# Kernel optimization log

Measured on AMD Instinct MI355X. Metric: run time of the kernel, lower is better.

## Reference

```python
import jax, jax.numpy as jnp
import numpy as np

HIDDEN = 64
EF_DIM = 3
RBOUND = 10.0
GROUP = 5
NEXP_MEAN = 0.05   # fixed normalization constants of the 'nexpnorm' RBF
NEXP_STD = 0.15
COORDS_WEIGHT = 1.0
N_NODES = 100000
N_GRAPHS = N_NODES // GROUP


def act(x):
    return jax.nn.relu(x)


def rbf(dist, num_rbf):
    # ExpNormal smearing with cosine cutoff (non-trainable), then fixed normalization.
    # dist: (..., 1) -> (..., num_rbf)
    alpha = 5.0 / RBOUND
    start = float(np.exp(-RBOUND))
    means = jnp.linspace(start, 1.0, num_rbf).astype(dist.dtype)
    beta = (2.0 / num_rbf * (1.0 - start)) ** -2
    cutoff = 0.5 * (jnp.cos(dist * jnp.pi / RBOUND) + 1.0) * (dist <= RBOUND)
    r = cutoff * jnp.exp(-beta * (jnp.exp(-alpha * dist) - means) ** 2)
    return (r - NEXP_MEAN) / NEXP_STD


def safe_pdist(a, b):
    # pairwise L2 norm (B,G,1,3)-(B,1,G,3) -> (B,G,G,1); grad-safe at zero
    d = a[:, :, None, :] - b[:, None, :, :]
    sq = jnp.sum(d * d, axis=-1, keepdims=True)
    return jnp.sqrt(jnp.where(sq == 0.0, 1.0, sq)) * (sq > 0.0)


def mlp2(x, w1, b1, w2, b2):
    return act(act(x @ w1 + b1) @ w2 + b2)


def mixed_wl(row, col, coord, vel, ic_wef, ic_pat, br_w1, br_b1, br_w2, br_b2, out_w, out_b):
    B = coord.shape[0] // GROUP
    c = coord.reshape(B, GROUP, 3)
    v = vel.reshape(B, GROUP, 3)
    mcd = safe_pdist(c, v)  # mixed coord-vel distances
    ef = jnp.concatenate([
        rbf(safe_pdist(c, c), EF_DIM),
        rbf(safe_pdist(v, v), EF_DIM),
        rbf(mcd, EF_DIM),
        rbf(jnp.swapaxes(mcd, 1, 2), EF_DIM),
    ], axis=-1)  # (B, 5, 5, 4*EF_DIM)
    # TwoFDisInit: linear embed * pattern embedding (diag tuples get pattern id 2, off-diag 1)
    idx = jnp.arange(GROUP)
    pattern = jnp.ones((GROUP, GROUP), dtype=jnp.int32).at[idx, idx].set(2)
    kemb = (ef @ ic_wef) * ic_pat[pattern]  # (B, 5, 5, H)
    # TwoFDisLayer (color_steps = 1): three branch MLPs, matrix-multiply mixing, residual add
    sm = mlp2(kemb, br_w1[0], br_b1[0], br_w2[0], br_b2[0])
    k0 = mlp2(kemb, br_w1[1], br_b1[1], br_w2[1], br_b2[1])
    k1 = mlp2(kemb, br_w1[2], br_b1[2], br_w2[2], br_b2[2])
    mult = jnp.einsum('bijd,bjkd->bikd', k0, k1)
    kemb = kemb + act((sm * mult) @ out_w + out_b)
    # gather per-edge tuple embedding
    return kemb[row // GROUP, row % GROUP, col % GROUP]  # (E, H)


def setup_inputs():
    key = jax.random.key(0)
    ks = jax.random.split(key, 20)
    N, H = N_NODES, HIDDEN
    # fully-connected (no self loops) edges inside each 5-node graph
    pairs = np.array([(i, j) for i in range(GROUP) for j in range(GROUP) if i != j])
    off = np.arange(N_GRAPHS) * GROUP
    row = (off[:, None] + pairs[None, :, 0]).reshape(-1)
    col = (off[:, None] + pairs[None, :, 1]).reshape(-1)
    edge_index = jnp.asarray(np.stack([row, col]), dtype=jnp.int32)
    g = lambda k, shp, s=0.05: jax.random.normal(k, shp, dtype=jnp.float32) * s
    return {
        'h': g(ks[0], (N, H), 0.5),
        'coord': g(ks[1], (N, 3), 1.0),
        'vel': g(ks[2], (N, 3), 1.0),
        'edge_index': edge_index,
        'e_w1': g(ks[3], (2 * H + 1 + H, H)), 'e_b1': jnp.zeros((H,), jnp.float32),
        'e_w2': g(ks[4], (H, H)), 'e_b2': jnp.zeros((H,), jnp.float32),
        'n_w1': g(ks[5], (2 * H, H)), 'n_b1': jnp.zeros((H,), jnp.float32),
        'n_w2': g(ks[6], (H, H)), 'n_b2': jnp.zeros((H,), jnp.float32),
        'c_w1': g(ks[7], (H, H)), 'c_b1': jnp.zeros((H,), jnp.float32),
        'c_w2': g(ks[8], (H, 1), 0.001),  # xavier gain=0.001, bias-free
        'v_w1': g(ks[9], (H, H)), 'v_b1': jnp.zeros((H,), jnp.float32),
        'v_w2': g(ks[10], (H, 1)), 'v_b2': jnp.zeros((1,), jnp.float32),
        'ic_wef': g(ks[11], (4 * EF_DIM, H), 0.1),
        'ic_pat': g(ks[12], (3, H), 0.1),
        'br_w1': g(ks[13], (3, H, H)), 'br_b1': jnp.zeros((3, H), jnp.float32),
        'br_w2': g(ks[14], (3, H, H)), 'br_b2': jnp.zeros((3, H), jnp.float32),
        'out_w': g(ks[15], (H, H)), 'out_b': jnp.zeros((H,), jnp.float32),
    }


def reference(h, coord, vel, edge_index, e_w1, e_b1, e_w2, e_b2, n_w1, n_b1, n_w2, n_b2,
              c_w1, c_b1, c_w2, v_w1, v_b1, v_w2, v_b2, ic_wef, ic_pat,
              br_w1, br_b1, br_w2, br_b2, out_w, out_b):
    row, col = edge_index[0], edge_index[1]
    N = h.shape[0]
    # coord2radial (norm_diff=False)
    coord_diff = coord[row] - coord[col]                      # (E, 3)
    radial = jnp.sum(coord_diff * coord_diff, axis=1, keepdims=True)  # (E, 1)
    # mixed 2-WL tuple embedding per edge
    kemb = mixed_wl(row, col, coord, vel, ic_wef, ic_pat, br_w1, br_b1, br_w2, br_b2, out_w, out_b)
    # edge model (attention=False)
    edge_feat = mlp2(jnp.concatenate([h[row], h[col], radial, kemb], axis=1),
                     e_w1, e_b1, e_w2, e_b2)                  # (E, H)
    # coord model: per-edge scalar (num_vectors_in=out=1), clamp, segment mean
    cmat = act(edge_feat @ c_w1 + c_b1) @ c_w2                # (E, 1)
    trans = jnp.clip(coord_diff * cmat, -100.0, 100.0)        # (E, 3)
    cnt = jax.ops.segment_sum(jnp.ones((row.shape[0],), trans.dtype), row, num_segments=N)
    agg = jax.ops.segment_sum(trans, row, num_segments=N) / jnp.maximum(cnt, 1.0)[:, None]
    # velocity update: coord += coord_mlp_vel(h) * vel
    vmat = act(h @ v_w1 + v_b1) @ v_w2 + v_b2                 # (N, 1)
    coord_out = (coord + agg * COORDS_WEIGHT + vel * vmat)[:, :, None]  # (N, 3, 1)
    # node model (recurrent=True)
    nagg = jax.ops.segment_sum(edge_feat, row, num_segments=N)
    h_out = h + (act(jnp.concatenate([h, nagg], axis=1) @ n_w1 + n_b1) @ n_w2 + n_b2)
    return h_out, coord_out
```

## Files before the change

### kernel.cpp

```cpp
#include <hip/hip_runtime.h>
#include <math.h>

#define HD 64
#define WPB 2

typedef unsigned short u16;
typedef unsigned int u32;
typedef __attribute__((ext_vector_type(8))) short short8;
typedef __attribute__((ext_vector_type(4))) float f32x4;

__device__ __forceinline__ u16 f2bf(float f) {
  u32 r;
  asm("v_cvt_pk_bf16_f32 %0, %1, %2" : "=v"(r) : "v"(f), "v"(f));
  return (u16)r;
}
__device__ __forceinline__ u32 pk2(float lo, float hi) {
  u32 r;
  asm("v_cvt_pk_bf16_f32 %0, %1, %2" : "=v"(r) : "v"(lo), "v"(hi));
  return r;
}
__device__ __forceinline__ float bf2f(u16 x) {
  return __uint_as_float(((u32)x) << 16);
}
__device__ __forceinline__ int uswz(int row, int col) {
  return (row << 6) | (col ^ (((row >> 2) & 3) << 4));
}
__device__ __forceinline__ float rlane(float v, int l) {
  return __uint_as_float(__builtin_amdgcn_readlane(__float_as_uint(v), l));
}
__device__ __forceinline__ void fence() {
  asm volatile("s_waitcnt lgkmcnt(0)" ::: "memory");
}

template <int MT, int RMAX>
__device__ __forceinline__ void loadA(const u16* A_, int t, short8* a0, short8* a1) {
  const int q8 = (t >> 4) << 3;
#pragma unroll
  for (int mt = 0; mt < MT; ++mt) {
    int row = mt * 16 + (t & 15);
    row = row > RMAX ? RMAX : row;
    const int idx = uswz(row, q8);
    a0[mt] = *reinterpret_cast<const short8*>(A_ + idx);
    a1[mt] = *reinterpret_cast<const short8*>(A_ + (idx ^ 32));
  }
}

template <int MTT>
__device__ __forceinline__ void mmh(const short8* a0, const short8* a1,
                                    const u16* __restrict__ WT, f32x4 (*acc)[2],
                                    int t, int nh) {
  const int c15 = t & 15;
  const int q8 = (t >> 4) << 3;
  short8 b[2][2];
#pragma unroll
  for (int n2 = 0; n2 < 2; ++n2) {
    const int nt = nh * 2 + n2;
#pragma unroll
    for (int s = 0; s < 2; ++s)
      b[n2][s] = *reinterpret_cast<const short8*>(WT + (nt * 16 + c15) * 64 + s * 32 + q8);
  }
#pragma unroll
  for (int mt = 0; mt < MTT; ++mt) {
#pragma unroll
    for (int n2 = 0; n2 < 2; ++n2)
      acc[mt][n2] = __builtin_amdgcn_mfma_f32_16x16x32_bf16(a0[mt], b[n2][0], acc[mt][n2], 0, 0, 0);
#pragma unroll
    for (int n2 = 0; n2 < 2; ++n2)
      acc[mt][n2] = __builtin_amdgcn_mfma_f32_16x16x32_bf16(a1[mt], b[n2][1], acc[mt][n2], 0, 0, 0);
  }
}

template <int MT, int RMAX, int EPI>
__device__ __forceinline__ void run_phase2(const u16* AA, const u16* AB,
                                           u16* DA, u16* DB,
                                           const u16* MA, const u16* MB,
                                           const u16* __restrict__ WT,
                                           const float* __restrict__ bias,
                                           int t, int rowoff = 0) {
  const int c15 = t & 15, q = t >> 4;
  constexpr int rowlim = (MT == 2) ? 25 : 5;
  short8 a0[2 * MT], a1[2 * MT];
  loadA<MT, RMAX>(AA, t, a0, a1);
  loadA<MT, RMAX>(AB, t, a0 + MT, a1 + MT);
#pragma unroll
  for (int nh = 0; nh < 2; ++nh) {
    f32x4 acc[2 * MT][2];
#pragma unroll
    for (int n2 = 0; n2 < 2; ++n2) {
      const int col = (nh * 2 + n2) * 16 + c15;
      const float bb = bias ? bias[col] : 0.0f;
#pragma unroll
      for (int mt = 0; mt < 2 * MT; ++mt) acc[mt][n2] = (f32x4){bb, bb, bb, bb};
    }
    mmh<2 * MT>(a0, a1, WT, acc, t, nh);
#pragma unroll
    for (int n2 = 0; n2 < 2; ++n2) {
      const int col = (nh * 2 + n2) * 16 + c15;
#pragma unroll
      for (int mt = 0; mt < 2 * MT; ++mt) {
        u16* D_ = (mt < MT) ? DA : DB;
        const u16* M_ = (mt < MT) ? MA : MB;
        const int r0 = (mt % MT) * 16 + q * 4;
        const int bix = uswz(r0 + rowoff, col);
#pragma unroll
        for (int i = 0; i < 4; ++i) {
          if (r0 + i < rowlim) {
            const int ix = bix + i * 64;
            float v = acc[mt][n2][i];
            if (EPI >= 2) v = fmaxf(v, 0.0f);
            if (EPI == 3) v *= bf2f(M_[ix]);
            if (EPI == 4) v += bf2f(D_[ix]);
            D_[ix] = f2bf(v);
          }
        }
      }
    }
  }
}

__global__ __launch_bounds__(256) void prepack(
    const float* __restrict__ br_w1, const float* __restrict__ br_w2,
    const float* __restrict__ out_w, const float* __restrict__ e_w1,
    const float* __restrict__ e_w2, const float* __restrict__ c_w1,
    const float* __restrict__ v_w1, const float* __restrict__ n_w1,
    const float* __restrict__ n_w2, const float* __restrict__ ic_wef,
    u16* __restrict__ W) {
  const int m = blockIdx.x;
  if (m == 16) {
    for (int e = threadIdx.x; e < 2048; e += blockDim.x) {
      const int n = e >> 5, k = e & 31;
      W[16 * 4096 + e] = (k < 12) ? f2bf(ic_wef[k * 64 + n]) : (u16)0;
    }
    return;
  }
  const float* src;
  switch (m) {
    case 0: src = br_w1; break;
    case 1: src = br_w1 + 4096; break;
    case 2: src = br_w1 + 8192; break;
    case 3: src = br_w2; break;
    case 4: src = br_w2 + 4096; break;
    case 5: src = br_w2 + 8192; break;
    case 6: src = out_w; break;
    case 7: src = e_w1; break;
    case 8: src = e_w1 + 64 * 64; break;
    case 9: src = e_w1 + 129 * 64; break;
    case 10: src = e_w2; break;
    case 11: src = c_w1; break;
    case 12: src = v_w1; break;
    case 13: src = n_w1; break;
    case 14: src = n_w1 + 64 * 64; break;
    default: src = n_w2; break;
  }
  u16* dst = W + m * 4096;
  for (int e = threadIdx.x; e < 4096; e += blockDim.x) {
    const int n = e >> 6, k = e & 63;
    dst[e] = f2bf(src[k * 64 + n]);
  }
}

__global__ __launch_bounds__(64 * WPB, 2) void egcl_mfma(
    const float* __restrict__ gh, const float* __restrict__ gcoord,
    const float* __restrict__ gvel, const u16* __restrict__ Wg,
    const float* __restrict__ e_w1, const float* __restrict__ e_b1,
    const float* __restrict__ e_b2,
    const float* __restrict__ n_b1, const float* __restrict__ n_b2,
    const float* __restrict__ c_b1, const float* __restrict__ c_w2,
    const float* __restrict__ v_b1, const float* __restrict__ v_w2,
    const float* __restrict__ v_b2,
    const float* __restrict__ ic_pat,
    const float* __restrict__ br_b1, const float* __restrict__ br_b2,
    const float* __restrict__ out_b,
    float* __restrict__ hout, float* __restrict__ cout, int B) {
  __shared__ __align__(16) u16 arena[WPB][9600];

  const int t = threadIdx.x & 63;
  const int wv = threadIdx.x >> 6;
  const int gA = (blockIdx.x * WPB + wv) * 2;
  if (gA >= B) return;
  int gB = gA + 1;
  if (gB >= B) gB = gA;

  u16* AR = arena[wv];
  u16* KA = AR;           u16* KB = AR + 1600;
  u16* TA = AR + 3200;    u16* TB = AR + 4800;
  u16* UA = AR + 6400;    u16* UB = AR + 8000;
  u16* EFa = TA;
  u16* EFb = TB;
  const int c15 = t & 15, q = t >> 4, q8 = q << 3;
#define WT(m) (Wg + (m) * 4096)

  short8 hA0, hA1;
  {
    int nd = c15 & 7;
    nd = nd > 4 ? 4 : nd;
    const int gg = (c15 & 8) ? gB : gA;
    const float* hp = gh + (size_t)(gg * 5 + nd) * HD + q8;
    const float4 f0 = *reinterpret_cast<const float4*>(hp);
    const float4 f1 = *reinterpret_cast<const float4*>(hp + 4);
    const float4 f2 = *reinterpret_cast<const float4*>(hp + 32);
    const float4 f3 = *reinterpret_cast<const float4*>(hp + 36);
    union { u32 w[4]; short8 s; } u0, u1;
    u0.w[0] = pk2(f0.x, f0.y); u0.w[1] = pk2(f0.z, f0.w);
    u0.w[2] = pk2(f1.x, f1.y); u0.w[3] = pk2(f1.z, f1.w);
    u1.w[0] = pk2(f2.x, f2.y); u1.w[1] = pk2(f2.z, f2.w);
    u1.w[2] = pk2(f3.x, f3.y); u1.w[3] = pk2(f3.z, f3.w);
    hA0 = u0.s;
    hA1 = u1.s;
  }

  float scvreg = 0.0f;
  if (t < 15) scvreg = gcoord[gA * 15 + t];
  else if (t >= 16 && t < 31) scvreg = gvel[gA * 15 + (t - 16)];
  else if (t >= 32 && t < 47) scvreg = gcoord[gB * 15 + (t - 32)];
  else if (t >= 48 && t < 63) scvreg = gvel[gB * 15 + (t - 48)];

#pragma unroll
  for (int z = 0; z < 8; ++z) {
    const int e = t + z * 64;
    if (e < 500) {
      const int gsel = e >= 250;
      const int ee = e - gsel * 250;
      const int row = ee / 10, cc = 12 + (ee % 10) * 2;
      *reinterpret_cast<u32*>((gsel ? EFb : EFa) + row * 32 + cc) = 0u;
    }
  }

  float sqcc = 0.0f;
  {
    const int lb = (t >= 32) ? 32 : 0;
    const int tt = t - lb;
    if (tt < 25) {
      u16* EF = lb ? EFb : EFa;
      const int ti = tt / 5, tj = tt % 5;
      const float cix = __shfl(scvreg, lb + ti * 3 + 0, 64), ciy = __shfl(scvreg, lb + ti * 3 + 1, 64), ciz = __shfl(scvreg, lb + ti * 3 + 2, 64);
      const float cjx = __shfl(scvreg, lb + tj * 3 + 0, 64), cjy = __shfl(scvreg, lb + tj * 3 + 1, 64), cjz = __shfl(scvreg, lb + tj * 3 + 2, 64);
      const float vix = __shfl(scvreg, lb + 16 + ti * 3 + 0, 64), viy = __shfl(scvreg, lb + 16 + ti * 3 + 1, 64), viz = __shfl(scvreg, lb + 16 + ti * 3 + 2, 64);
      const float vjx = __shfl(scvreg, lb + 16 + tj * 3 + 0, 64), vjy = __shfl(scvreg, lb + 16 + tj * 3 + 1, 64), vjz = __shfl(scvreg, lb + 16 + tj * 3 + 2, 64);
      {
        const float dx = cix - cjx, dy = ciy - cjy, dz = ciz - cjz;
        sqcc = dx * dx + dy * dy + dz * dz;
      }
      auto sd = [](float sq) { return (sq > 0.0f) ? sqrtf(sq) : 0.0f; };
      float sq2;
      const float dcc = sd(sqcc);
      {
        const float dx = vix - vjx, dy = viy - vjy, dz = viz - vjz;
        sq2 = dx * dx + dy * dy + dz * dz;
      }
      const float dvv = sd(sq2);
      {
        const float dx = cix - vjx, dy = ciy - vjy, dz = ciz - vjz;
        sq2 = dx * dx + dy * dy + dz * dz;
      }
      const float dcv = sd(sq2);
      {
        const float dx = cjx - vix, dy = cjy - viy, dz = cjz - viz;
        sq2 = dx * dx + dy * dy + dz * dz;
      }
      const float dvc = sd(sq2);
      auto rbf3 = [&](float d, int base) {
        const float cut = (d <= 10.0f) ? (0.5f * (cosf(d * 0.31415926535897931f) + 1.0f)) : 0.0f;
        const float e = expf(-0.5f * d);
        const float u0 = e - 4.5399929762484854e-05f;
        const float u1 = e - 0.50002270f;
        const float u2 = e - 1.0f;
        const float BETA = 2.2502043f;
        EF[tt * 32 + base + 0] = f2bf((cut * expf(-BETA * u0 * u0) - 0.05f) * (1.0f / 0.15f));
        EF[tt * 32 + base + 1] = f2bf((cut * expf(-BETA * u1 * u1) - 0.05f) * (1.0f / 0.15f));
        EF[tt * 32 + base + 2] = f2bf((cut * expf(-BETA * u2 * u2) - 0.05f) * (1.0f / 0.15f));
      };
      rbf3(dcc, 0);
      rbf3(dvv, 3);
      rbf3(dcv, 6);
      rbf3(dvc, 9);
    }
  }
  fence();

  {
    short8 aE[4];
#pragma unroll
    for (int gsel = 0; gsel < 2; ++gsel) {
      const u16* EF = gsel ? EFb : EFa;
#pragma unroll
      for (int mt = 0; mt < 2; ++mt) {
        int row = mt * 16 + c15;
        row = row > 24 ? 24 : row;
        aE[gsel * 2 + mt] = *reinterpret_cast<const short8*>(EF + row * 32 + q8);
      }
    }
    const u16* WTp = Wg + 16 * 4096;
#pragma unroll
    for (int nh = 0; nh < 2; ++nh) {
      f32x4 acc[4][2];
#pragma unroll
      for (int mt = 0; mt < 4; ++mt)
#pragma unroll
        for (int n2 = 0; n2 < 2; ++n2) acc[mt][n2] = (f32x4){0.f, 0.f, 0.f, 0.f};
      short8 b[2];
#pragma unroll
      for (int n2 = 0; n2 < 2; ++n2)
        b[n2] = *reinterpret_cast<const short8*>(WTp + ((nh * 2 + n2) * 16 + c15) * 32 + q8);
#pragma unroll
      for (int mt = 0; mt < 4; ++mt)
#pragma unroll
        for (int n2 = 0; n2 < 2; ++n2)
          acc[mt][n2] = __builtin_amdgcn_mfma_f32_16x16x32_bf16(aE[mt], b[n2], acc[mt][n2], 0, 0, 0);
#pragma unroll
      for (int n2 = 0; n2 < 2; ++n2) {
        const int col = (nh * 2 + n2) * 16 + c15;
        const float p1 = ic_pat[64 + col], p2 = ic_pat[128 + col];
#pragma unroll
        for (int mt = 0; mt < 4; ++mt) {
          u16* K_ = (mt < 2) ? KA : KB;
          const int r0 = (mt & 1) * 16 + q * 4;
          const int bix = uswz(r0, col);
#pragma unroll
          for (int i = 0; i < 4; ++i) {
            const int row = r0 + i;
            if (row < 25) {
              const bool diag = (row % 6) == 0;
              K_[bix + i * 64] = f2bf(acc[mt][n2][i] * (diag ? p2 : p1));
            }
          }
        }
      }
    }
  }
  fence();

  {
    short8 a0[4], a1[4];
    loadA<2, 24>(KA, t, a0, a1);
    loadA<2, 24>(KB, t, a0 + 2, a1 + 2);
#pragma unroll
    for (int nh = 0; nh < 2; ++nh) {
      f32x4 ac0[4][2], ac1[4][2];
#pragma unroll
      for (int n2 = 0; n2 < 2; ++n2) {
        const int col = (nh * 2 + n2) * 16 + c15;
        const float b0 = br_b1[64 + col], b1 = br_b1[128 + col];
#pragma unroll
        for (int mt = 0; mt < 4; ++mt) {
          ac0[mt][n2] = (f32x4){b0, b0, b0, b0};
          ac1[mt][n2] = (f32x4){b1, b1, b1, b1};
        }
      }
      mmh<4>(a0, a1, WT(1), ac0, t, nh);
      mmh<4>(a0, a1, WT(2), ac1, t, nh);
#pragma unroll
      for (int n2 = 0; n2 < 2; ++n2) {
        const int col = (nh * 2 + n2) * 16 + c15;
#pragma unroll
        for (int mt = 0; mt < 4; ++mt) {
          u16* T_ = (mt < 2) ? TA : TB;
          u16* U_ = (mt < 2) ? UA : UB;
          const int r0 = (mt & 1) * 16 + q * 4;
          const int bix = uswz(r0, col);
#pragma unroll
          for (int i = 0; i < 4; ++i) {
            if (r0 + i < 25) {
              T_[bix + i * 64] = f2bf(fmaxf(ac0[mt][n2][i], 0.0f));
              U_[bix + i * 64] = f2bf(fmaxf(ac1[mt][n2][i], 0.0f));
            }
          }
        }
      }
    }
  }
  fence();

  {
    short8 a0[4], a1[4], c0[4], c1[4];
    loadA<2, 24>(TA, t, a0, a1);
    loadA<2, 24>(TB, t, a0 + 2, a1 + 2);
    loadA<2, 24>(UA, t, c0, c1);
    loadA<2, 24>(UB, t, c0 + 2, c1 + 2);
#pragma unroll
    for (int nh = 0; nh < 2; ++nh) {
      f32x4 ac0[4][2], ac1[4][2];
#pragma unroll
      for (int n2 = 0; n2 < 2; ++n2) {
        const int col = (nh * 2 + n2) * 16 + c15;
        const float b0 = br_b2[64 + col], b1 = br_b2[128 + col];
#pragma unroll
        for (int mt = 0; mt < 4; ++mt) {
          ac0[mt][n2] = (f32x4){b0, b0, b0, b0};
          ac1[mt][n2] = (f32x4){b1, b1, b1, b1};
        }
      }
      mmh<4>(a0, a1, WT(4), ac0, t, nh);
      mmh<4>(c0, c1, WT(5), ac1, t, nh);
#pragma unroll
      for (int n2 = 0; n2 < 2; ++n2) {
        const int col = (nh * 2 + n2) * 16 + c15;
#pragma unroll
        for (int mt = 0; mt < 4; ++mt) {
          u16* T_ = (mt < 2) ? TA : TB;
          u16* U_ = (mt < 2) ? UA : UB;
          const int r0 = (mt & 1) * 16 + q * 4;
          const int bix = uswz(r0, col);
#pragma unroll
          for (int i = 0; i < 4; ++i) {
            if (r0 + i < 25) {
              T_[bix + i * 64] = f2bf(fmaxf(ac0[mt][n2][i], 0.0f));
              U_[bix + i * 64] = f2bf(fmaxf(ac1[mt][n2][i], 0.0f));
            }
          }
        }
      }
    }
  }
  fence();

  {
    float mu[2][25];
#pragma unroll
    for (int gsel = 0; gsel < 2; ++gsel)
#pragma unroll
      for (int p = 0; p < 25; ++p) mu[gsel][p] = 0.0f;
#pragma unroll
    for (int j = 0; j < 5; ++j) {
#pragma unroll
      for (int gsel = 0; gsel < 2; ++gsel) {
        const u16* Tg = gsel ? TB : TA;
        const u16* Ug = gsel ? UB : UA;
        float k1r[5], k0c[5];
#pragma unroll
        for (int k = 0; k < 5; ++k) k1r[k] = bf2f(Ug[uswz(j * 5 + k, t)]);
#pragma unroll
        for (int i = 0; i < 5; ++i) k0c[i] = bf2f(Tg[uswz(i * 5 + j, t)]);
#pragma unroll
        for (int i = 0; i < 5; ++i)
#pragma unroll
          for (int k = 0; k < 5; ++k)
            mu[gsel][i * 5 + k] = fmaf(k0c[i], k1r[k], mu[gsel][i * 5 + k]);
      }
    }
    fence();
#pragma unroll
    for (int p = 0; p < 25; ++p) {
      UA[uswz(p, t)] = f2bf(mu[0][p]);
      UB[uswz(p, t)] = f2bf(mu[1][p]);
    }
  }
  fence();

  run_phase2<2, 24, 2>(KA, KB, TA, TB, nullptr, nullptr, WT(0), br_b1, t); fence();
  run_phase2<2, 24, 3>(TA, TB, TA, TB, UA, UB, WT(3), br_b2, t); fence();
  run_phase2<2, 24, 4>(TA, TB, KA, KB, nullptr, nullptr, WT(6), out_b, t); fence();

  float svv[4];
  {
    short8 a0[4], a1[4];
    loadA<2, 24>(KA, t, a0, a1);
    loadA<2, 24>(KB, t, a0 + 2, a1 + 2);
    float s[4] = {0.f, 0.f, 0.f, 0.f};
#pragma unroll
    for (int nh = 0; nh < 2; ++nh) {
      f32x4 accC[4][2], aA[1][2], aB[1][2], aV[1][2];
#pragma unroll
      for (int n2 = 0; n2 < 2; ++n2) {
        const float bv = v_b1[(nh * 2 + n2) * 16 + c15];
#pragma unroll
        for (int mt = 0; mt < 4; ++mt) accC[mt][n2] = (f32x4){0.f, 0.f, 0.f, 0.f};
        aA[0][n2] = (f32x4){0.f, 0.f, 0.f, 0.f};
        aB[0][n2] = (f32x4){0.f, 0.f, 0.f, 0.f};
        aV[0][n2] = (f32x4){bv, bv, bv, bv};
      }
      mmh<4>(a0, a1, WT(9), accC, t, nh);
      mmh<1>(&hA0, &hA1, WT(7), aA, t, nh);
      mmh<1>(&hA0, &hA1, WT(8), aB, t, nh);
      mmh<1>(&hA0, &hA1, WT(12), aV, t, nh);
#pragma unroll
      for (int n2 = 0; n2 < 2; ++n2) {
        const int col = (nh * 2 + n2) * 16 + c15;
        const float w2v = v_w2[col];
#pragma unroll
        for (int mt = 0; mt < 4; ++mt) {
          u16* T_ = (mt < 2) ? TA : TB;
          const int r0 = (mt & 1) * 16 + q * 4;
          const int bix = uswz(r0, col);
#pragma unroll
          for (int i = 0; i < 4; ++i)
            if (r0 + i < 25) T_[bix + i * 64] = f2bf(accC[mt][n2][i]);
        }
#pragma unroll
        for (int i = 0; i < 4; ++i) {
          const int r = q * 4 + i;
          if (r < 5) {
            UA[uswz(r, col)] = f2bf(aA[0][n2][i]);
            UA[uswz(r + 8, col)] = f2bf(aB[0][n2][i]);
          } else if (r >= 8 && r < 13) {
            UB[uswz(r - 8, col)] = f2bf(aA[0][n2][i]);
            UB[uswz(r, col)] = f2bf(aB[0][n2][i]);
          }
          s[i] += fmaxf(aV[0][n2][i], 0.0f) * w2v;
        }
      }
    }
#pragma unroll
    for (int i = 0; i < 4; ++i) {
      float ss = s[i];
      ss += __shfl_xor(ss, 1, 64);
      ss += __shfl_xor(ss, 2, 64);
      ss += __shfl_xor(ss, 4, 64);
      ss += __shfl_xor(ss, 8, 64);
      svv[i] = ss;
    }
  }
  fence();

  {
    float ec[2][20];
#pragma unroll
    for (int gsel = 0; gsel < 2; ++gsel) {
      const int lb = gsel * 32;
      const u16* Ug = gsel ? UB : UA;
      const u16* Tg = gsel ? TB : TA;
      float aAc[5], aBc[5];
#pragma unroll
      for (int i = 0; i < 5; ++i) {
        aAc[i] = bf2f(Ug[uswz(i, t)]);
        aBc[i] = bf2f(Ug[uswz(8 + i, t)]);
      }
      const float eb1v = e_b1[t];
      const float wradv = e_w1[128 * HD + t];
#pragma unroll
      for (int p = 0; p < 20; ++p) {
        const int i = p >> 2, jj = p & 3;
        const int j = jj + (jj >= i ? 1 : 0);
        const float radial = rlane(sqcc, lb + i * 5 + j);
        const float cc = bf2f(Tg[uswz(i * 5 + j, t)]);
        ec[gsel][p] = fmaxf(aAc[i] + aBc[j] + radial * wradv + cc + eb1v, 0.0f);
      }
    }
    fence();
#pragma unroll
    for (int p = 0; p < 20; ++p) {
      TA[uswz(p, t)] = f2bf(ec[0][p]);
      TB[uswz(p, t)] = f2bf(ec[1][p]);
    }
  }
  fence();

  {
    short8 a0[4], a1[4];
    loadA<2, 24>(TA, t, a0, a1);
    loadA<2, 24>(TB, t, a0 + 2, a1 + 2);
#pragma unroll
    for (int nh = 0; nh < 2; ++nh) {
      f32x4 acc[4][2];
#pragma unroll
      for (int n2 = 0; n2 < 2; ++n2) {
        const float bb = e_b2[(nh * 2 + n2) * 16 + c15];
#pragma unroll
        for (int mt = 0; mt < 4; ++mt) acc[mt][n2] = (f32x4){bb, bb, bb, bb};
      }
      mmh<4>(a0, a1, WT(10), acc, t, nh);
#pragma unroll
      for (int n2 = 0; n2 < 2; ++n2) {
        const int col = (nh * 2 + n2) * 16 + c15;
#pragma unroll
        for (int mt = 0; mt < 4; ++mt) {
          u16* U_ = (mt < 2) ? UA : UB;
          const int gsel = mt >> 1;
          const int r0 = (mt & 1) * 16 + q * 4;
          const int bix = uswz(r0, col);
          float na = 0.0f;
#pragma unroll
          for (int i = 0; i < 4; ++i) {
            const float v = fmaxf(acc[mt][n2][i], 0.0f);
            if (r0 + i < 25) U_[bix + i * 64] = f2bf(v);
            na += v;
          }
          if (!(mt & 1)) {
            KA[uswz(gsel * 8 + q, col)] = f2bf(na);
          } else if (q == 0) {
            KA[uswz(gsel * 8 + 4, col)] = f2bf(na);
          }
        }
      }
    }
  }
  fence();

  float svc[4][4];
  {
    short8 u0[4], u1[4], k0[1], k1[1];
    loadA<2, 24>(UA, t, u0, u1);
    loadA<2, 24>(UB, t, u0 + 2, u1 + 2);
    loadA<1, 15>(KA, t, k0, k1);
    float s[4][4];
#pragma unroll
    for (int mt = 0; mt < 4; ++mt)
#pragma unroll
      for (int i = 0; i < 4; ++i) s[mt][i] = 0.0f;
#pragma unroll
    for (int nh = 0; nh < 2; ++nh) {
      f32x4 accc[4][2], accn[1][2];
#pragma unroll
      for (int n2 = 0; n2 < 2; ++n2) {
        const int col = (nh * 2 + n2) * 16 + c15;
        const float bv = c_b1[col];
        const float nb = n_b1[col];
#pragma unroll
        for (int mt = 0; mt < 4; ++mt) accc[mt][n2] = (f32x4){bv, bv, bv, bv};
        accn[0][n2] = (f32x4){nb, nb, nb, nb};
      }
      mmh<4>(u0, u1, WT(11), accc, t, nh);
      mmh<1>(&hA0, &hA1, WT(13), accn, t, nh);
      mmh<1>(k0, k1, WT(14), accn, t, nh);
#pragma unroll
      for (int n2 = 0; n2 < 2; ++n2) {
        const int col = (nh * 2 + n2) * 16 + c15;
        const float w2v = c_w2[col];
#pragma unroll
        for (int mt = 0; mt < 4; ++mt)
#pragma unroll
          for (int i = 0; i < 4; ++i)
            s[mt][i] += fmaxf(accc[mt][n2][i], 0.0f) * w2v;
#pragma unroll
        for (int i = 0; i < 4; ++i) {
          const int r = q * 4 + i;
          if (r < 5 || (r >= 8 && r < 13))
            TA[uswz(r, col)] = f2bf(fmaxf(accn[0][n2][i], 0.0f));
        }
      }
    }
#pragma unroll
    for (int mt = 0; mt < 4; ++mt)
#pragma unroll
      for (int i = 0; i < 4; ++i) {
        float ss = s[mt][i];
        ss += __shfl_xor(ss, 1, 64);
        ss += __shfl_xor(ss, 2, 64);
        ss += __shfl_xor(ss, 4, 64);
        ss += __shfl_xor(ss, 8, 64);
        svc[mt][i] = ss;
      }
  }
  fence();

  {
    const float vb2 = v_b2[0];
    float coutreg = 0.0f;
#pragma unroll
    for (int gsel = 0; gsel < 2; ++gsel) {
      const int lb = gsel * 32;
#pragma unroll
      for (int i = 0; i < 5; ++i) {
        const int rr = gsel * 8 + i;
        const float vmi = rlane(svv[rr & 3], (rr >> 2) << 4) + vb2;
#pragma unroll
        for (int dd = 0; dd < 3; ++dd) {
          const float ci = rlane(scvreg, lb + i * 3 + dd);
          float s = 0.0f;
#pragma unroll
          for (int jj = 0; jj < 4; ++jj) {
            const int j = jj + (jj >= i ? 1 : 0);
            const int p = i * 4 + jj;
            const float cmp = rlane(svc[gsel * 2 + (p >> 4)][p & 3], ((p & 15) >> 2) << 4);
            float tr = (ci - rlane(scvreg, lb + j * 3 + dd)) * cmp;
            tr = fminf(fmaxf(tr, -100.0f), 100.0f);
            s += tr;
          }
          const float val = ci + 0.25f * s + rlane(scvreg, lb + 16 + i * 3 + dd) * vmi;
          if (t == lb + i * 3 + dd) coutreg = val;
        }
      }
    }
    if (t < 15) cout[gA * 15 + t] = coutreg;
    else if (t >= 32 && t < 47) cout[gB * 15 + (t - 32)] = coutreg;
  }

  {
    short8 a0[1], a1[1];
    loadA<1, 15>(TA, t, a0, a1);
#pragma unroll
    for (int nh = 0; nh < 2; ++nh) {
      f32x4 acc[1][2];
#pragma unroll
      for (int n2 = 0; n2 < 2; ++n2) {
        const float nb = n_b2[(nh * 2 + n2) * 16 + c15];
        acc[0][n2] = (f32x4){nb, nb, nb, nb};
      }
      mmh<1>(a0, a1, WT(15), acc, t, nh);
#pragma unroll
      for (int n2 = 0; n2 < 2; ++n2) {
        const int col = (nh * 2 + n2) * 16 + c15;
#pragma unroll
        for (int i = 0; i < 4; ++i) {
          const int r = q * 4 + i;
          if (r < 5) {
            const size_t ix = (size_t)(gA * 5 + r) * HD + col;
            hout[ix] = gh[ix] + acc[0][n2][i];
          } else if (r >= 8 && r < 13) {
            const size_t ix = (size_t)(gB * 5 + (r - 8)) * HD + col;
            hout[ix] = gh[ix] + acc[0][n2][i];
          }
        }
      }
    }
  }
#undef WT
}

extern "C" void kernel_launch(void* const* d_in, const int* in_sizes, int n_in,
                              void* d_out, int out_size, void* d_ws, size_t ws_size,
                              hipStream_t stream) {
  if (n_in < 27) return;
  const float* gh    = (const float*)d_in[0];
  const float* coord = (const float*)d_in[1];
  const float* vel   = (const float*)d_in[2];
  const float* e_w1 = (const float*)d_in[4];
  const float* e_b1 = (const float*)d_in[5];
  const float* e_w2 = (const float*)d_in[6];
  const float* e_b2 = (const float*)d_in[7];
  const float* n_w1 = (const float*)d_in[8];
  const float* n_b1 = (const float*)d_in[9];
  const float* n_w2 = (const float*)d_in[10];
  const float* n_b2 = (const float*)d_in[11];
  const float* c_w1 = (const float*)d_in[12];
  const float* c_b1 = (const float*)d_in[13];
  const float* c_w2 = (const float*)d_in[14];
  const float* v_w1 = (const float*)d_in[15];
  const float* v_b1 = (const float*)d_in[16];
  const float* v_w2 = (const float*)d_in[17];
  const float* v_b2 = (const float*)d_in[18];
  const float* ic_wef = (const float*)d_in[19];
  const float* ic_pat = (const float*)d_in[20];
  const float* br_w1 = (const float*)d_in[21];
  const float* br_b1 = (const float*)d_in[22];
  const float* br_w2 = (const float*)d_in[23];
  const float* br_b2 = (const float*)d_in[24];
  const float* out_w = (const float*)d_in[25];
  const float* out_b = (const float*)d_in[26];

  const int N = in_sizes[0] / HD;
  const int B = N / 5;
  float* hout = (float*)d_out;
  float* cout = (float*)d_out + (size_t)N * HD;
  u16* W = (u16*)d_ws;

  prepack<<<17, 256, 0, stream>>>(br_w1, br_w2, out_w, e_w1, e_w2, c_w1, v_w1,
                                  n_w1, n_w2, ic_wef, W);

  const int gpb = WPB * 2;
  const int blocks = (B + gpb - 1) / gpb;
  egcl_mfma<<<blocks, 64 * WPB, 0, stream>>>(
      gh, coord, vel, W, e_w1, e_b1, e_b2, n_b1, n_b2, c_b1, c_w2, v_b1, v_w2,
      v_b2, ic_pat, br_b1, br_b2, out_b, hout, cout, B);
}
```

Measured before the change: 237.4 us.

## Raise wave priority around MFMA blocks and vectorize coord epilogue per lane

Wraps every MFMA block in s_setprio(1)/s_setprio(0) so that waves issuing matrix ops are favoured by the scheduler over waves doing memory or epilogue work. The coordinate-update epilogue used to be a fully unrolled loop over all 30 outputs, where every lane ran every cross-lane read and kept only its own result. It now computes one output per lane, using a handful of __shfl calls chosen by lane index. This removes many redundant rlane broadcasts but adds dynamic shuffles and selects.

```diff
diff --git a/kernel.cpp b/kernel.cpp
--- a/kernel.cpp
+++ b/kernel.cpp
@@ -92,7 +92,9 @@
 #pragma unroll
       for (int mt = 0; mt < 2 * MT; ++mt) acc[mt][n2] = (f32x4){bb, bb, bb, bb};
     }
+    __builtin_amdgcn_s_setprio(1);
     mmh<2 * MT>(a0, a1, WT, acc, t, nh);
+    __builtin_amdgcn_s_setprio(0);
 #pragma unroll
     for (int n2 = 0; n2 < 2; ++n2) {
       const int col = (nh * 2 + n2) * 16 + c15;
@@ -302,11 +304,13 @@
 #pragma unroll
       for (int n2 = 0; n2 < 2; ++n2)
         b[n2] = *reinterpret_cast<const short8*>(WTp + ((nh * 2 + n2) * 16 + c15) * 32 + q8);
+      __builtin_amdgcn_s_setprio(1);
 #pragma unroll
       for (int mt = 0; mt < 4; ++mt)
 #pragma unroll
         for (int n2 = 0; n2 < 2; ++n2)
           acc[mt][n2] = __builtin_amdgcn_mfma_f32_16x16x32_bf16(aE[mt], b[n2], acc[mt][n2], 0, 0, 0);
+      __builtin_amdgcn_s_setprio(0);
 #pragma unroll
       for (int n2 = 0; n2 < 2; ++n2) {
         const int col = (nh * 2 + n2) * 16 + c15;
@@ -347,8 +351,10 @@
           ac1[mt][n2] = (f32x4){b1, b1, b1, b1};
         }
       }
+      __builtin_amdgcn_s_setprio(1);
       mmh<4>(a0, a1, WT(1), ac0, t, nh);
       mmh<4>(a0, a1, WT(2), ac1, t, nh);
+      __builtin_amdgcn_s_setprio(0);
 #pragma unroll
       for (int n2 = 0; n2 < 2; ++n2) {
         const int col = (nh * 2 + n2) * 16 + c15;
@@ -390,8 +396,10 @@
           ac1[mt][n2] = (f32x4){b1, b1, b1, b1};
         }
       }
+      __builtin_amdgcn_s_setprio(1);
       mmh<4>(a0, a1, WT(4), ac0, t, nh);
       mmh<4>(c0, c1, WT(5), ac1, t, nh);
+      __builtin_amdgcn_s_setprio(0);
 #pragma unroll
       for (int n2 = 0; n2 < 2; ++n2) {
         const int col = (nh * 2 + n2) * 16 + c15;
@@ -469,10 +477,12 @@
         aB[0][n2] = (f32x4){0.f, 0.f, 0.f, 0.f};
         aV[0][n2] = (f32x4){bv, bv, bv, bv};
       }
+      __builtin_amdgcn_s_setprio(1);
       mmh<4>(a0, a1, WT(9), accC, t, nh);
       mmh<1>(&hA0, &hA1, WT(7), aA, t, nh);
       mmh<1>(&hA0, &hA1, WT(8), aB, t, nh);
       mmh<1>(&hA0, &hA1, WT(12), aV, t, nh);
+      __builtin_amdgcn_s_setprio(0);
 #pragma unroll
       for (int n2 = 0; n2 < 2; ++n2) {
         const int col = (nh * 2 + n2) * 16 + c15;
@@ -558,7 +568,9 @@
 #pragma unroll
         for (int mt = 0; mt < 4; ++mt) acc[mt][n2] = (f32x4){bb, bb, bb, bb};
       }
+      __builtin_amdgcn_s_setprio(1);
       mmh<4>(a0, a1, WT(10), acc, t, nh);
+      __builtin_amdgcn_s_setprio(0);
 #pragma unroll
       for (int n2 = 0; n2 < 2; ++n2) {
         const int col = (nh * 2 + n2) * 16 + c15;
@@ -586,7 +598,7 @@
   }
   fence();
 
-  float svc[4][4];
+  float svcA[2][4], svcB[2][4];
   {
     short8 u0[4], u1[4], k0[1], k1[1];
     loadA<2, 24>(UA, t, u0, u1);
@@ -609,9 +621,11 @@
         for (int mt = 0; mt < 4; ++mt) accc[mt][n2] = (f32x4){bv, bv, bv, bv};
         accn[0][n2] = (f32x4){nb, nb, nb, nb};
       }
+      __builtin_amdgcn_s_setprio(1);
       mmh<4>(u0, u1, WT(11), accc, t, nh);
       mmh<1>(&hA0, &hA1, WT(13), accn, t, nh);
       mmh<1>(k0, k1, WT(14), accn, t, nh);
+      __builtin_amdgcn_s_setprio(0);
 #pragma unroll
       for (int n2 = 0; n2 < 2; ++n2) {
         const int col = (nh * 2 + n2) * 16 + c15;
@@ -638,41 +652,51 @@
         ss += __shfl_xor(ss, 2, 64);
         ss += __shfl_xor(ss, 4, 64);
         ss += __shfl_xor(ss, 8, 64);
-        svc[mt][i] = ss;
+        if (mt < 2) svcA[mt][i] = ss; else svcB[mt - 2][i] = ss;
       }
   }
   fence();
 
   {
     const float vb2 = v_b2[0];
-    float coutreg = 0.0f;
-#pragma unroll
-    for (int gsel = 0; gsel < 2; ++gsel) {
-      const int lb = gsel * 32;
-#pragma unroll
-      for (int i = 0; i < 5; ++i) {
-        const int rr = gsel * 8 + i;
-        const float vmi = rlane(svv[rr & 3], (rr >> 2) << 4) + vb2;
-#pragma unroll
-        for (int dd = 0; dd < 3; ++dd) {
-          const float ci = rlane(scvreg, lb + i * 3 + dd);
-          float s = 0.0f;
-#pragma unroll
-          for (int jj = 0; jj < 4; ++jj) {
-            const int j = jj + (jj >= i ? 1 : 0);
-            const int p = i * 4 + jj;
-            const float cmp = rlane(svc[gsel * 2 + (p >> 4)][p & 3], ((p & 15) >> 2) << 4);
-            float tr = (ci - rlane(scvreg, lb + j * 3 + dd)) * cmp;
-            tr = fminf(fmaxf(tr, -100.0f), 100.0f);
-            s += tr;
-          }
-          const float val = ci + 0.25f * s + rlane(scvreg, lb + 16 + i * 3 + dd) * vmi;
-          if (t == lb + i * 3 + dd) coutreg = val;
-        }
-      }
-    }
-    if (t < 15) cout[gA * 15 + t] = coutreg;
-    else if (t >= 32 && t < 47) cout[gB * 15 + (t - 32)] = coutreg;
+    const int lb = (t >= 32) ? 32 : 0;
+    const int tt = t - lb;
+    const int gsel = lb ? 1 : 0;
+    int ii = tt / 3;
+    if (ii > 4) ii = 4;
+    const int dd = tt - (tt / 3) * 3;
+    const int rr = gsel * 8 + ii;
+    const int sl = (rr >> 2) << 4;
+    const float w0 = __shfl(svv[0], sl, 64);
+    const float w1 = __shfl(svv[1], sl, 64);
+    const float w2 = __shfl(svv[2], sl, 64);
+    const float w3 = __shfl(svv[3], sl, 64);
+    float vsel = w0;
+    vsel = ((rr & 3) == 1) ? w1 : vsel;
+    vsel = ((rr & 3) == 2) ? w2 : vsel;
+    vsel = ((rr & 3) == 3) ? w3 : vsel;
+    const float vmi = vsel + vb2;
+    const float ci = scvreg;
+    const float vel_ = __shfl(scvreg, lb + 16 + tt, 64);
+    const bool i4 = (ii == 4);
+    const int cl = i4 ? 0 : (ii << 4);
+    float ssum = 0.0f;
+#pragma unroll
+    for (int jj = 0; jj < 4; ++jj) {
+      const int j = jj + (jj >= ii ? 1 : 0);
+      const float a0 = __shfl(svcA[0][jj], cl, 64);
+      const float a1 = __shfl(svcA[1][jj], cl, 64);
+      const float b0 = __shfl(svcB[0][jj], cl, 64);
+      const float b1 = __shfl(svcB[1][jj], cl, 64);
+      const float cmp = gsel ? (i4 ? b1 : b0) : (i4 ? a1 : a0);
+      const float cj = __shfl(scvreg, lb + j * 3 + dd, 64);
+      float tr = (ci - cj) * cmp;
+      tr = fminf(fmaxf(tr, -100.0f), 100.0f);
+      ssum += tr;
+    }
+    const float val = ci + 0.25f * ssum + vel_ * vmi;
+    if (t < 15) cout[gA * 15 + t] = val;
+    else if (t >= 32 && t < 47) cout[gB * 15 + (t - 32)] = val;
   }
 
   {
@@ -686,7 +710,9 @@
         const float nb = n_b2[(nh * 2 + n2) * 16 + c15];
         acc[0][n2] = (f32x4){nb, nb, nb, nb};
       }
+      __builtin_amdgcn_s_setprio(1);
       mmh<1>(a0, a1, WT(15), acc, t, nh);
+      __builtin_amdgcn_s_setprio(0);
 #pragma unroll
       for (int n2 = 0; n2 < 2; ++n2) {
         const int col = (nh * 2 + n2) * 16 + c15;
```

Result: no change. 236.8 us (median of 2 runs) (-0.3%).
